# Optimization experiments

Measured on AMD Instinct MI355X. Metric: run time of the kernel, lower is better.

## Reference

```python
import jax, jax.numpy as jnp
import numpy as np

B_, L_, D_ = 8, 2048, 1024      # batch, seq_len, d_model
E, DS, K = 2, 16, 4             # expand, d_state, d_conv
DI = E * D_                     # d_inner = 2048
DTR = (D_ + 15) // 16           # dt_rank = 64


def setup_inputs() -> dict:
    key = jax.random.key(0)
    ks = jax.random.split(key, 8)
    g = lambda k, sh, sc=0.02: jax.random.normal(k, sh, jnp.float32) * sc
    return {
        "x": jax.random.normal(ks[0], (B_, L_, D_), jnp.float32),
        "ln_w": jnp.ones((D_,), jnp.float32),
        "ln_b": jnp.zeros((D_,), jnp.float32),
        "W_in": g(ks[1], (D_, 2 * DI)),
        "conv_w": g(ks[2], (DI, 1, K), 0.1),
        "conv_b": jnp.zeros((DI,), jnp.float32),
        "W_x": g(ks[3], (DI, DTR + 2 * DS)),
        "W_dt": g(ks[4], (DTR, DI), 0.1),
        "b_dt": jnp.full((DI,), -4.0, jnp.float32),  # softplus(-4) ~ 0.018 (small init dt)
        "A_log": jnp.log(jnp.broadcast_to(jnp.arange(1, DS + 1, dtype=jnp.float32), (DI, DS))),
        "Dp": jnp.ones((DI,), jnp.float32),
        "W_out": g(ks[5], (DI, D_)),
    }


def _mamba_block(x, ln_w, ln_b, W_in, conv_w, conv_b, W_x, W_dt, b_dt, A_log, Dp, W_out):
    # pre-norm
    mu = jnp.mean(x, axis=-1, keepdims=True)
    var = jnp.var(x, axis=-1, keepdims=True)
    xn = (x - mu) / jnp.sqrt(var + 1e-5) * ln_w + ln_b

    # input projection -> (u, z), each (B, L, DI)
    xz = jnp.einsum('bld,de->ble', xn, W_in)
    u, z = jnp.split(xz, 2, axis=-1)

    # causal depthwise conv1d along L
    uc = jax.lax.conv_general_dilated(
        u.transpose(0, 2, 1), conv_w, window_strides=(1,), padding=[(K - 1, 0)],
        feature_group_count=DI, dimension_numbers=('NCH', 'OIH', 'NCH'))
    u = jax.nn.silu(uc.transpose(0, 2, 1) + conv_b)

    # input-dependent SSM params
    xd = jnp.einsum('bld,de->ble', u, W_x)          # (B, L, DTR + 2*DS)
    dt = jax.nn.softplus(jnp.einsum('blr,rd->bld', xd[..., :DTR], W_dt) + b_dt)  # (B, L, DI)
    Bm = xd[..., DTR:DTR + DS]                       # (B, L, DS)
    Cm = xd[..., DTR + DS:]                          # (B, L, DS)
    A = -jnp.exp(A_log)                              # (DI, DS)

    # selective scan over time; carry h: (B, DI, DS)
    def step(h, inp):
        dt_t, u_t, B_t, C_t = inp                    # (B,DI),(B,DI),(B,DS),(B,DS)
        dA = jnp.exp(dt_t[..., None] * A)            # (B, DI, DS)
        h = h * dA + (dt_t * u_t)[..., None] * B_t[:, None, :]
        y = jnp.einsum('bds,bs->bd', h, C_t)
        return h, y

    h0 = jnp.zeros((x.shape[0], DI, DS), x.dtype)
    xs = (dt.transpose(1, 0, 2), u.transpose(1, 0, 2), Bm.transpose(1, 0, 2), Cm.transpose(1, 0, 2))
    _, ys = jax.lax.scan(step, h0, xs)               # ys: (L, B, DI)

    y = ys.transpose(1, 0, 2) + u * Dp
    y = y * jax.nn.silu(z)
    # output projection + residual (dropout is identity in eval)
    return jnp.einsum('bld,de->ble', y, W_out) + x


def reference(x, ln_w, ln_b, W_in, conv_w, conv_b, W_x, W_dt, b_dt, A_log, Dp, W_out):
    return _mamba_block(x, ln_w, ln_b, W_in, conv_w, conv_b, W_x, W_dt, b_dt, A_log, Dp, W_out)
```

## Files before the change

### kernel.cpp

```cpp
#include <hip/hip_runtime.h>

#define NB 8
#define NL 2048
#define ND 1024
#define NDI 2048
#define NDS 16
#define NDTR 64
#define NM (NB * NL)
#define CH 16
#define CL (NL / CH)

__device__ __forceinline__ float bf2f(unsigned int u) {
  union { unsigned int i; float f; } c; c.i = u << 16; return c.f;
}
__device__ __forceinline__ float lo16(unsigned int w) { return __uint_as_float(w << 16); }
__device__ __forceinline__ float hi16(unsigned int w) { return __uint_as_float(w & 0xffff0000u); }
__device__ __forceinline__ unsigned short f2bf(float f) {
  unsigned int x = __float_as_uint(f);
  x = x + 0x7fffu + ((x >> 16) & 1u);
  return (unsigned short)(x >> 16);
}
__device__ __forceinline__ void dec8(int4 raw, float* f) {
  f[0] = lo16((unsigned)raw.x); f[1] = hi16((unsigned)raw.x);
  f[2] = lo16((unsigned)raw.y); f[3] = hi16((unsigned)raw.y);
  f[4] = lo16((unsigned)raw.z); f[5] = hi16((unsigned)raw.z);
  f[6] = lo16((unsigned)raw.w); f[7] = hi16((unsigned)raw.w);
}
__device__ __forceinline__ float softplus_fast(float x) {
  return fmaxf(x, 0.f) + __logf(1.f + __expf(-fabsf(x)));
}

typedef __bf16 bf16x8 __attribute__((ext_vector_type(8)));
typedef float f32x4 __attribute__((ext_vector_type(4)));

__device__ __forceinline__ void gld_lds16(const unsigned short* g, unsigned short* l) {
  __builtin_amdgcn_global_load_lds(
      (const __attribute__((address_space(1))) unsigned int*)g,
      (__attribute__((address_space(3))) unsigned int*)l, 16, 0, 0);
}

__global__ __launch_bounds__(256) void k_ln(const float* __restrict__ x,
    const float* __restrict__ lw, const float* __restrict__ lb,
    unsigned short* __restrict__ xn)
{
  const int row = blockIdx.x;
  const int tid = threadIdx.x;
  const float* xr = x + (size_t)row * ND;
  float4 v = reinterpret_cast<const float4*>(xr)[tid];
  float s  = v.x + v.y + v.z + v.w;
  float s2 = v.x*v.x + v.y*v.y + v.z*v.z + v.w*v.w;
  #pragma unroll
  for (int m = 32; m >= 1; m >>= 1) {
    s  += __shfl_xor(s, m);
    s2 += __shfl_xor(s2, m);
  }
  __shared__ float red[8];
  const int wid = tid >> 6;
  if ((tid & 63) == 0) { red[wid] = s; red[4 + wid] = s2; }
  __syncthreads();
  s  = red[0] + red[1] + red[2] + red[3];
  s2 = red[4] + red[5] + red[6] + red[7];
  const float mu   = s * (1.0f / ND);
  const float var  = s2 * (1.0f / ND) - mu * mu;
  const float rstd = rsqrtf(var + 1e-5f);
  const float4 wv = reinterpret_cast<const float4*>(lw)[tid];
  const float4 bv = reinterpret_cast<const float4*>(lb)[tid];
  ushort4 o;
  o.x = f2bf((v.x - mu) * rstd * wv.x + bv.x);
  o.y = f2bf((v.y - mu) * rstd * wv.y + bv.y);
  o.z = f2bf((v.z - mu) * rstd * wv.z + bv.z);
  o.w = f2bf((v.w - mu) * rstd * wv.w + bv.w);
  reinterpret_cast<ushort4*>(xn + (size_t)row * ND)[tid] = o;
}

__global__ __launch_bounds__(256) void k_transpose(
    const float* __restrict__ W, unsigned short* __restrict__ WT,
    const int K, const int N)
{
  __shared__ float t[32][33];
  const int k0 = blockIdx.y * 32, n0 = blockIdx.x * 32;
  const int tx = threadIdx.x & 31, ty = threadIdx.x >> 5;
  #pragma unroll
  for (int r = 0; r < 4; ++r)
    t[ty + r * 8][tx] = W[(size_t)(k0 + ty + r * 8) * N + n0 + tx];
  __syncthreads();
  #pragma unroll
  for (int r = 0; r < 4; ++r)
    WT[(size_t)(n0 + ty + r * 8) * K + k0 + tx] = f2bf(t[tx][ty + r * 8]);
}

template<int MODE>
__global__ __launch_bounds__(512, 2) void k_mfma2(
    const unsigned short* __restrict__ A, const unsigned short* __restrict__ BT,
    const int K, const int N, void* __restrict__ O0, void* __restrict__ O1,
    const float* __restrict__ aux)
{
  __shared__ __align__(16) unsigned short sh[32768];
  const int tid = threadIdx.x, lane = tid & 63, wv = tid >> 6;
  const int wm = wv >> 2, wn = wv & 3;
  const int m16 = lane & 15, kb = lane >> 4;
  const int swzs = (((kb * 16) ^ (((m16 >> 1) & 3) << 4)) >> 1);
  const int arow = wm * 128 + m16;
  const int brow = wn * 64 + m16;

  int wg = blockIdx.x;
  const int cpx = gridDim.x >> 3;
  wg = (wg & 7) * cpx + (wg >> 3);
  const int gnx = N >> 8;
  const int m0 = (wg / gnx) << 8;
  const int n0 = (wg % gnx) << 8;

  f32x4 acc[8][4];
  #pragma unroll
  for (int i = 0; i < 8; ++i)
    #pragma unroll
    for (int j = 0; j < 4; ++j)
      #pragma unroll
      for (int r = 0; r < 4; ++r) acc[i][j][r] = 0.f;

  auto STAGE = [&](const unsigned short* X, int x0, int kg, unsigned short* base) {
    #pragma unroll
    for (int jj = 0; jj < 2; ++jj) {
      const int s = (wv * 2 + jj) * 64 + lane;
      const int row = s >> 2;
      const int c = (lane & 3) ^ ((row >> 1) & 3);
      gld_lds16(X + (size_t)(x0 + row) * K + kg + c * 8, base + (wv * 2 + jj) * 512);
    }
  };
  auto RD_A = [&](bf16x8* dst, const unsigned short* base, int FH) {
    #pragma unroll
    for (int i = 0; i < 4; ++i)
      dst[i] = *reinterpret_cast<const bf16x8*>(base + (arow + FH * 64 + i * 16) * 32 + swzs);
  };
  auto RD_B = [&](bf16x8* dst, const unsigned short* base) {
    #pragma unroll
    for (int j = 0; j < 4; ++j)
      dst[j] = *reinterpret_cast<const bf16x8*>(base + (brow + j * 16) * 32 + swzs);
  };
  auto MM = [&](const bf16x8* aF, const bf16x8* bF, int off) {
    #pragma unroll
    for (int i = 0; i < 4; ++i)
      #pragma unroll
      for (int j = 0; j < 4; ++j)
        acc[off + i][j] = __builtin_amdgcn_mfma_f32_16x16x32_bf16(aF[i], bF[j], acc[off + i][j], 0, 0, 0);
  };

  STAGE(A,  m0, 0, sh);
  STAGE(BT, n0, 0, sh + 8192);
  asm volatile("s_waitcnt vmcnt(0)" ::: "memory");
  __builtin_amdgcn_s_barrier();

  const int NT = K >> 5;
  for (int t = 0; t < NT; ++t) {
    const int buf = t & 1;
    const unsigned short* cA = sh + buf * 16384;
    const unsigned short* cB = cA + 8192;
    unsigned short* nA = sh + (buf ^ 1) * 16384;
    const bool more = (t + 1 < NT);
    if (more) {
      const int kn = (t + 1) << 5;
      STAGE(A,  m0, kn, nA);
      STAGE(BT, n0, kn, nA + 8192);
    }
    bf16x8 a0[4], a1[4], bF[4];
    RD_A(a0, cA, 0);
    RD_B(bF, cB);
    RD_A(a1, cA, 1);
    __builtin_amdgcn_sched_barrier(0);
    __builtin_amdgcn_s_setprio(1);
    MM(a0, bF, 0);
    MM(a1, bF, 4);
    __builtin_amdgcn_s_setprio(0);
    if (more) asm volatile("s_waitcnt vmcnt(0)" ::: "memory");
    __builtin_amdgcn_s_barrier();
  }

  {
    float* fsh = (float*)sh;
    constexpr int LDP = 260;
    const int erow = tid >> 4;
    const int ec0  = tid & 15;
    const int growb = m0 + (erow >> 4) * 128 + (erow & 15);
    #pragma unroll
    for (int i = 0; i < 8; ++i) {
      __builtin_amdgcn_s_barrier();
      #pragma unroll
      for (int j = 0; j < 4; ++j)
        #pragma unroll
        for (int r = 0; r < 4; ++r)
          fsh[(wm * 16 + kb * 4 + r) * LDP + wn * 64 + j * 16 + m16] = acc[i][j][r];
      __builtin_amdgcn_s_barrier();
      const int grow = growb + i * 16;
      #pragma unroll
      for (int q = 0; q < 4; ++q) {
        const int c = (ec0 + q * 16) * 4;
        float4 v = *reinterpret_cast<const float4*>(&fsh[erow * LDP + c]);
        const int colg = n0 + c;
        if constexpr (MODE == 0) {
          ushort4 o = {f2bf(v.x), f2bf(v.y), f2bf(v.z), f2bf(v.w)};
          unsigned short* dst = (colg < NDI)
              ? (unsigned short*)O0 + (size_t)grow * NDI + colg
              : (unsigned short*)O1 + (size_t)grow * NDI + colg - NDI;
          *reinterpret_cast<ushort4*>(dst) = o;
        } else {
          float4 rv = *reinterpret_cast<const float4*>(aux + (size_t)grow * N + colg);
          float4 o = {v.x + rv.x, v.y + rv.y, v.z + rv.z, v.w + rv.w};
          *reinterpret_cast<float4*>((float*)O0 + (size_t)grow * N + colg) = o;
        }
      }
    }
  }
  (void)O1; (void)aux;
}

__global__ __launch_bounds__(256) void k_mfma_dt(
    const unsigned short* __restrict__ A, const unsigned short* __restrict__ BT,
    const int K, void* __restrict__ O0, const float* __restrict__ aux, const int N)
{
  __shared__ __align__(16) unsigned short As[128 * 32];
  __shared__ __align__(16) unsigned short Bs[128 * 32];
  const int tid = threadIdx.x;
  const int lane = tid & 63;
  const int wv = tid >> 6;
  const int wm = wv >> 1, wn = wv & 1;
  const int m0 = blockIdx.y * 128, n0 = blockIdx.x * 128;
  const int m16 = lane & 15, kb = lane >> 4;
  const int wbase = wv * 64;

  f32x4 acc[4][4];
  #pragma unroll
  for (int i = 0; i < 4; ++i)
    #pragma unroll
    for (int j = 0; j < 4; ++j)
      #pragma unroll
      for (int r = 0; r < 4; ++r) acc[i][j][r] = 0.f;

  for (int k0 = 0; k0 < K; k0 += 32) {
    #pragma unroll
    for (int it = 0; it < 2; ++it) {
      const int c = it * 256 + tid;
      const int r = c >> 2, cb = c & 3;
      gld_lds16(A  + (size_t)(m0 + r) * K + k0 + cb * 8, As + (size_t)(it * 256 + wbase) * 8);
      gld_lds16(BT + (size_t)(n0 + r) * K + k0 + cb * 8, Bs + (size_t)(it * 256 + wbase) * 8);
    }
    __syncthreads();
    bf16x8 af[4], bfr[4];
    #pragma unroll
    for (int i = 0; i < 4; ++i)
      af[i] = *reinterpret_cast<const bf16x8*>(&As[(wm * 64 + i * 16 + m16) * 32 + kb * 8]);
    #pragma unroll
    for (int j = 0; j < 4; ++j)
      bfr[j] = *reinterpret_cast<const bf16x8*>(&Bs[(wn * 64 + j * 16 + m16) * 32 + kb * 8]);
    #pragma unroll
    for (int i = 0; i < 4; ++i)
      #pragma unroll
      for (int j = 0; j < 4; ++j)
        acc[i][j] = __builtin_amdgcn_mfma_f32_16x16x32_bf16(af[i], bfr[j], acc[i][j], 0, 0, 0);
    __syncthreads();
  }

  const int r0 = (lane >> 4) * 4;
  #pragma unroll
  for (int i = 0; i < 4; ++i) {
    const int rowb = m0 + wm * 64 + i * 16 + r0;
    #pragma unroll
    for (int j = 0; j < 4; ++j) {
      const int col = n0 + wn * 64 + j * 16 + m16;
      #pragma unroll
      for (int r = 0; r < 4; ++r) {
        const int row = rowb + r;
        ((unsigned short*)O0)[(size_t)row * N + col] =
            f2bf(softplus_fast(acc[i][j][r] + aux[col]));
      }
    }
  }
}

__global__ __launch_bounds__(256) void k_conv(
    const unsigned short* __restrict__ up, const float* __restrict__ cw,
    const float* __restrict__ cb, unsigned short* __restrict__ u)
{
  const int tid = threadIdx.x;
  const int c0 = tid * 8;
  const int lt = blockIdx.x & 127;
  const int b  = blockIdx.x >> 7;
  const int l0 = lt * 16;

  float4 wv[8];
  #pragma unroll
  for (int j = 0; j < 8; ++j)
    wv[j] = reinterpret_cast<const float4*>(cw + (size_t)c0 * 4)[j];
  float bias[8];
  {
    float4 b0 = reinterpret_cast<const float4*>(cb + c0)[0];
    float4 b1 = reinterpret_cast<const float4*>(cb + c0)[1];
    bias[0]=b0.x; bias[1]=b0.y; bias[2]=b0.z; bias[3]=b0.w;
    bias[4]=b1.x; bias[5]=b1.y; bias[6]=b1.z; bias[7]=b1.w;
  }

  const size_t base = ((size_t)b * NL + l0) * NDI + c0;
  float w0[8], w1[8], w2[8];
  if (l0 >= 3) {
    int4 r0 = *reinterpret_cast<const int4*>(up + base - 3 * NDI);
    int4 r1 = *reinterpret_cast<const int4*>(up + base - 2 * NDI);
    int4 r2 = *reinterpret_cast<const int4*>(up + base - 1 * NDI);
    dec8(r0, w0); dec8(r1, w1); dec8(r2, w2);
  } else {
    #pragma unroll
    for (int j = 0; j < 8; ++j) { w0[j] = 0.f; w1[j] = 0.f; w2[j] = 0.f; }
  }

  #pragma unroll
  for (int l = 0; l < 16; ++l) {
    int4 raw = *reinterpret_cast<const int4*>(up + base + (size_t)l * NDI);
    float cur[8];
    dec8(raw, cur);
    unsigned short o[8];
    #pragma unroll
    for (int j = 0; j < 8; ++j) {
      const float a = bias[j] + wv[j].x * w0[j] + wv[j].y * w1[j]
                              + wv[j].z * w2[j] + wv[j].w * cur[j];
      o[j] = f2bf(a / (1.f + __expf(-a)));
    }
    ushort4 o0 = {o[0], o[1], o[2], o[3]};
    ushort4 o1 = {o[4], o[5], o[6], o[7]};
    unsigned short* dst = u + base + (size_t)l * NDI;
    *reinterpret_cast<ushort4*>(dst)     = o0;
    *reinterpret_cast<ushort4*>(dst + 4) = o1;
    #pragma unroll
    for (int j = 0; j < 8; ++j) { w0[j] = w1[j]; w1[j] = w2[j]; w2[j] = cur[j]; }
  }
}

__global__ __launch_bounds__(256) void k_xd_mfma(
    const unsigned short* __restrict__ A, const unsigned short* __restrict__ BT,
    unsigned short* __restrict__ xdt, float* __restrict__ xb,
    float* __restrict__ xc)
{
  __shared__ __align__(16) unsigned short As[2][64 * 32];
  __shared__ __align__(16) unsigned short Bs[2][96 * 32];
  const int tid = threadIdx.x, lane = tid & 63, wvv = tid >> 6;
  const int m0 = blockIdx.x * 64;
  const int m16 = lane & 15, kb = lane >> 4;
  const int sw = (kb ^ ((m16 >> 1) & 3)) * 8;

  f32x4 acc[6];
  #pragma unroll
  for (int j = 0; j < 6; ++j)
    #pragma unroll
    for (int r = 0; r < 4; ++r) acc[j][r] = 0.f;

  auto STG = [&](int bb, int kg) {
    {
      const int row = tid >> 2, c = tid & 3;
      const int sc = c ^ ((row >> 1) & 3);
      gld_lds16(A + (size_t)(m0 + row) * NDI + kg + sc * 8, &As[bb][tid * 8]);
      gld_lds16(BT + (size_t)row * NDI + kg + sc * 8, &Bs[bb][tid * 8]);
    }
    if (tid < 128) {
      const int s = 256 + tid;
      const int row = s >> 2, c = s & 3;
      const int sc = c ^ ((row >> 1) & 3);
      gld_lds16(BT + (size_t)row * NDI + kg + sc * 8, &Bs[bb][s * 8]);
    }
  };

  STG(0, 0);
  asm volatile("s_waitcnt vmcnt(0)" ::: "memory");
  __syncthreads();

  for (int t = 0; t < NDI / 32; ++t) {
    const int cur = t & 1;
    if (t + 1 < NDI / 32) STG(cur ^ 1, (t + 1) * 32);
    bf16x8 af = *reinterpret_cast<const bf16x8*>(&As[cur][(wvv * 16 + m16) * 32 + sw]);
    bf16x8 bfr[6];
    #pragma unroll
    for (int j = 0; j < 6; ++j)
      bfr[j] = *reinterpret_cast<const bf16x8*>(&Bs[cur][(j * 16 + m16) * 32 + sw]);
    #pragma unroll
    for (int j = 0; j < 6; ++j)
      acc[j] = __builtin_amdgcn_mfma_f32_16x16x32_bf16(af, bfr[j], acc[j], 0, 0, 0);
    asm volatile("s_waitcnt vmcnt(0)" ::: "memory");
    __syncthreads();
  }

  const int r0 = kb * 4;
  #pragma unroll
  for (int j = 0; j < 6; ++j) {
    const int col = j * 16 + m16;
    #pragma unroll
    for (int r = 0; r < 4; ++r) {
      const int row = m0 + wvv * 16 + r0 + r;
      const float v = acc[j][r];
      if (j < 4)       xdt[(size_t)row * 64 + col] = f2bf(v);
      else if (j == 4) xb[(size_t)row * 16 + col - 64] = v;
      else             xc[(size_t)row * 16 + col - 80] = v;
    }
  }
}

template<int PHASE>
__global__ __launch_bounds__(256) void k_scan3(
    const unsigned short* __restrict__ dt, unsigned short* __restrict__ u_io,
    const unsigned short* __restrict__ z,
    const float* __restrict__ xb, const float* __restrict__ xc,
    const float* __restrict__ A_log, const float* __restrict__ Dp,
    float* __restrict__ HF, float* __restrict__ Sdt)
{
  const int tid = threadIdx.x;
  const int blk = blockIdx.x;
  const int b = blk >> 7;
  const int c = (blk >> 3) & (CH - 1);
  if (PHASE == 0 && c == CH - 1) return;
  const int d = (blk & 7) * 256 + tid;

  __shared__ float Bsl[CL][16];
  __shared__ float Csl[(PHASE == 1) ? CL : 1][16];
  const size_t rbase = (size_t)b * NL + (size_t)c * CL;
  #pragma unroll
  for (int i = 0; i < 2; ++i) {
    const int idx = i * 256 + tid;
    const int r = idx >> 2, q = idx & 3;
    reinterpret_cast<float4*>(&Bsl[r][q * 4])[0] =
        reinterpret_cast<const float4*>(xb + (rbase + r) * 16)[q];
    if constexpr (PHASE == 1)
      reinterpret_cast<float4*>(&Csl[r][q * 4])[0] =
          reinterpret_cast<const float4*>(xc + (rbase + r) * 16)[q];
  }
  __syncthreads();

  float Ac[16];
  #pragma unroll
  for (int q = 0; q < 4; ++q) {
    float4 a = reinterpret_cast<const float4*>(A_log + (size_t)d * 16)[q];
    Ac[q*4+0] = -__expf(a.x); Ac[q*4+1] = -__expf(a.y);
    Ac[q*4+2] = -__expf(a.z); Ac[q*4+3] = -__expf(a.w);
  }
  bool fastok = true;
  #pragma unroll
  for (int s = 1; s < 16; ++s)
    fastok = fastok && (fabsf(Ac[s] - Ac[0] * (float)(s + 1)) <= 1e-5f * fabsf(Ac[s]));
  const bool fast = __all(fastok);

  const size_t hoff = ((size_t)(b * CH + c) * NDI + d) * 16;
  float h[16];
  if constexpr (PHASE == 0) {
    #pragma unroll
    for (int s = 0; s < 16; ++s) h[s] = 0.f;
  } else {
    #pragma unroll
    for (int q = 0; q < 4; ++q) {
      float4 hv = reinterpret_cast<const float4*>(HF + hoff)[q];
      h[q*4+0] = hv.x; h[q*4+1] = hv.y; h[q*4+2] = hv.z; h[q*4+3] = hv.w;
    }
  }
  const float Dd = Dp[d];
  const float Ac0 = Ac[0];
  float sdt = 0.f;
  size_t idx = rbase * NDI + d;

  if (fast) {
    for (int l = 0; l < CL; ++l, idx += NDI) {
      const float dtv = bf2f(dt[idx]);
      const float uv  = bf2f(u_io[idx]);
      const float dtu = dtv * uv;
      const float qq = __expf(dtv * Ac0);
      float e = qq;
      if constexpr (PHASE == 0) {
        sdt += dtv;
        #pragma unroll
        for (int s = 0; s < 16; ++s) {
          h[s] = h[s] * e + dtu * Bsl[l][s];
          e *= qq;
        }
      } else {
        float yp = 0.f;
        #pragma unroll
        for (int s = 0; s < 16; ++s) {
          h[s] = h[s] * e + dtu * Bsl[l][s];
          yp += h[s] * Csl[l][s];
          e *= qq;
        }
        const float zv = bf2f(z[idx]);
        const float sil = zv / (1.f + __expf(-zv));
        u_io[idx] = f2bf((yp + uv * Dd) * sil);
      }
    }
  } else {
    for (int l = 0; l < CL; ++l, idx += NDI) {
      const float dtv = bf2f(dt[idx]);
      const float uv  = bf2f(u_io[idx]);
      const float dtu = dtv * uv;
      if constexpr (PHASE == 0) {
        sdt += dtv;
        #pragma unroll
        for (int s = 0; s < 16; ++s) {
          const float e = __expf(dtv * Ac[s]);
          h[s] = h[s] * e + dtu * Bsl[l][s];
        }
      } else {
        float yp = 0.f;
        #pragma unroll
        for (int s = 0; s < 16; ++s) {
          const float e = __expf(dtv * Ac[s]);
          h[s] = h[s] * e + dtu * Bsl[l][s];
          yp += h[s] * Csl[l][s];
        }
        const float zv = bf2f(z[idx]);
        const float sil = zv / (1.f + __expf(-zv));
        u_io[idx] = f2bf((yp + uv * Dd) * sil);
      }
    }
  }

  if constexpr (PHASE == 0) {
    #pragma unroll
    for (int q = 0; q < 4; ++q) {
      float4 hv = {h[q*4+0], h[q*4+1], h[q*4+2], h[q*4+3]};
      reinterpret_cast<float4*>(HF + hoff)[q] = hv;
    }
    Sdt[(size_t)(b * CH + c) * NDI + d] = sdt;
  }
}

__global__ __launch_bounds__(256) void k_comb(
    float* __restrict__ HF, const float* __restrict__ Sdt,
    const float* __restrict__ A_log)
{
  const int t = blockIdx.x * 256 + threadIdx.x;
  const int b = t >> 15;
  const int q = t & 32767;
  const int d = q >> 4;
  const float Ac = -__expf(A_log[q]);
  float H = 0.f;
  #pragma unroll
  for (int c = 0; c < CH; ++c) {
    const size_t off = (((size_t)(b * CH + c) * NDI) << 4) + q;
    const float hf = HF[off];
    const float p  = __expf(Ac * Sdt[(size_t)(b * CH + c) * NDI + d]);
    HF[off] = H;
    H = p * H + hf;
  }
}

extern "C" void kernel_launch(void* const* d_in, const int* in_sizes, int n_in,
                              void* d_out, int out_size, void* d_ws, size_t ws_size,
                              hipStream_t stream) {
  (void)in_sizes; (void)n_in; (void)out_size; (void)ws_size;
  const float* x      = (const float*)d_in[0];
  const float* ln_w   = (const float*)d_in[1];
  const float* ln_b   = (const float*)d_in[2];
  const float* W_in   = (const float*)d_in[3];
  const float* conv_w = (const float*)d_in[4];
  const float* conv_b = (const float*)d_in[5];
  const float* W_x    = (const float*)d_in[6];
  const float* W_dt   = (const float*)d_in[7];
  const float* b_dt   = (const float*)d_in[8];
  const float* A_log  = (const float*)d_in[9];
  const float* Dp     = (const float*)d_in[10];
  const float* W_out  = (const float*)d_in[11];
  float* out = (float*)d_out;

  char* ws = (char*)d_ws;
  unsigned short* xn   = (unsigned short*)(ws);
  float*          HF   = (float*)(ws);
  unsigned short* upre = (unsigned short*)(ws + 33554432);
  unsigned short* zbuf = (unsigned short*)(ws + 100663296);
  unsigned short* ubuf = (unsigned short*)(ws + 167772160);
  unsigned short* xdt  = (unsigned short*)(ws + 234881024);
  float*          Sdt  = (float*)(ws + 234881024);
  float*          xb   = (float*)(ws + 236978176);
  float*          xc   = (float*)(ws + 238026752);
  unsigned short* WxT  = (unsigned short*)(ws + 239075328);
  unsigned short* WdtT = (unsigned short*)(ws + 239468544);
  unsigned short* WinT = (unsigned short*)(ws + 240123904);
  unsigned short* WoutT= (unsigned short*)(ws + 248512512);

  dim3 gt1(4096 / 32, 1024 / 32);
  k_transpose<<<gt1, 256, 0, stream>>>(W_in, WinT, 1024, 4096);
  dim3 gt2(1024 / 32, 2048 / 32);
  k_transpose<<<gt2, 256, 0, stream>>>(W_out, WoutT, 2048, 1024);
  dim3 gt3(96 / 32, 2048 / 32);
  k_transpose<<<gt3, 256, 0, stream>>>(W_x, WxT, 2048, 96);
  dim3 gt4(2048 / 32, 64 / 32);
  k_transpose<<<gt4, 256, 0, stream>>>(W_dt, WdtT, 64, 2048);

  k_ln<<<NM, 256, 0, stream>>>(x, ln_w, ln_b, xn);

  k_mfma2<0><<<(NM / 256) * (4096 / 256), 512, 0, stream>>>(
      xn, WinT, 1024, 4096, upre, zbuf, nullptr);

  k_conv<<<NB * (NL / 16), 256, 0, stream>>>(upre, conv_w, conv_b, ubuf);

  k_xd_mfma<<<NM / 64, 256, 0, stream>>>(ubuf, WxT, xdt, xb, xc);

  dim3 g3(2048 / 128, NM / 128);
  k_mfma_dt<<<g3, 256, 0, stream>>>(xdt, WdtT, 64, upre, b_dt, 2048);

  const int nscan = NB * CH * (NDI / 256);
  k_scan3<0><<<nscan, 256, 0, stream>>>(upre, ubuf, zbuf, xb, xc, A_log, Dp, HF, Sdt);
  k_comb<<<NB * NDI * NDS / 256, 256, 0, stream>>>(HF, Sdt, A_log);
  k_scan3<1><<<nscan, 256, 0, stream>>>(upre, ubuf, zbuf, xb, xc, A_log, Dp, HF, Sdt);

  k_mfma2<1><<<(NM / 256) * (1024 / 256), 512, 0, stream>>>(
      ubuf, WoutT, 2048, 1024, out, nullptr, x);
}
```

Before: 540.8 us.

## Shrink GEMM tile to 128x256 for higher occupancy and coalesce dt epilogue

The main bf16 MFMA GEMM moves from a 256x256 tile to a 128x256 tile. This halves the accumulator registers and cuts LDS per block, so launch bounds rise to four blocks per CU and the grid doubles. In exchange each block reuses its staged B data across fewer rows, so arithmetic intensity drops. The dt-projection kernel's epilogue now goes through shared memory and writes vectorized ushort4 rows instead of scattered 2-byte stores, at the cost of extra barriers and LDS.

Result: no change. 550.4 us (+1.8%).

```diff
diff --git a/kernel.cpp b/kernel.cpp
--- a/kernel.cpp
+++ b/kernel.cpp
@@ -90,86 +90,81 @@
 }
 
 template<int MODE>
-__global__ __launch_bounds__(512, 2) void k_mfma2(
+__global__ __launch_bounds__(512, 4) void k_mfma3(
     const unsigned short* __restrict__ A, const unsigned short* __restrict__ BT,
     const int K, const int N, void* __restrict__ O0, void* __restrict__ O1,
     const float* __restrict__ aux)
 {
-  __shared__ __align__(16) unsigned short sh[32768];
+  __shared__ __align__(16) unsigned short sh[24576];
   const int tid = threadIdx.x, lane = tid & 63, wv = tid >> 6;
   const int wm = wv >> 2, wn = wv & 3;
   const int m16 = lane & 15, kb = lane >> 4;
   const int swzs = (((kb * 16) ^ (((m16 >> 1) & 3) << 4)) >> 1);
-  const int arow = wm * 128 + m16;
+  const int arow = wm * 64 + m16;
   const int brow = wn * 64 + m16;
 
   int wg = blockIdx.x;
   const int cpx = gridDim.x >> 3;
   wg = (wg & 7) * cpx + (wg >> 3);
   const int gnx = N >> 8;
-  const int m0 = (wg / gnx) << 8;
+  const int m0 = (wg / gnx) << 7;
   const int n0 = (wg % gnx) << 8;
 
-  f32x4 acc[8][4];
-  #pragma unroll
-  for (int i = 0; i < 8; ++i)
+  f32x4 acc[4][4];
+  #pragma unroll
+  for (int i = 0; i < 4; ++i)
     #pragma unroll
     for (int j = 0; j < 4; ++j)
       #pragma unroll
       for (int r = 0; r < 4; ++r) acc[i][j][r] = 0.f;
 
-  auto STAGE = [&](const unsigned short* X, int x0, int kg, unsigned short* base) {
+  auto STAGE_A = [&](int kg, unsigned short* base) {
+    const int s = wv * 64 + lane;
+    const int row = s >> 2;
+    const int c = (s & 3) ^ ((row >> 1) & 3);
+    gld_lds16(A + (size_t)(m0 + row) * K + kg + c * 8, base + wv * 512);
+  };
+  auto STAGE_B = [&](int kg, unsigned short* base) {
     #pragma unroll
     for (int jj = 0; jj < 2; ++jj) {
       const int s = (wv * 2 + jj) * 64 + lane;
       const int row = s >> 2;
-      const int c = (lane & 3) ^ ((row >> 1) & 3);
-      gld_lds16(X + (size_t)(x0 + row) * K + kg + c * 8, base + (wv * 2 + jj) * 512);
+      const int c = (s & 3) ^ ((row >> 1) & 3);
+      gld_lds16(BT + (size_t)(n0 + row) * K + kg + c * 8, base + (wv * 2 + jj) * 512);
     }
   };
-  auto RD_A = [&](bf16x8* dst, const unsigned short* base, int FH) {
-    #pragma unroll
-    for (int i = 0; i < 4; ++i)
-      dst[i] = *reinterpret_cast<const bf16x8*>(base + (arow + FH * 64 + i * 16) * 32 + swzs);
-  };
-  auto RD_B = [&](bf16x8* dst, const unsigned short* base) {
-    #pragma unroll
-    for (int j = 0; j < 4; ++j)
-      dst[j] = *reinterpret_cast<const bf16x8*>(base + (brow + j * 16) * 32 + swzs);
-  };
-  auto MM = [&](const bf16x8* aF, const bf16x8* bF, int off) {
-    #pragma unroll
-    for (int i = 0; i < 4; ++i)
-      #pragma unroll
-      for (int j = 0; j < 4; ++j)
-        acc[off + i][j] = __builtin_amdgcn_mfma_f32_16x16x32_bf16(aF[i], bF[j], acc[off + i][j], 0, 0, 0);
-  };
-
-  STAGE(A,  m0, 0, sh);
-  STAGE(BT, n0, 0, sh + 8192);
+
+  STAGE_A(0, sh);
+  STAGE_B(0, sh + 4096);
   asm volatile("s_waitcnt vmcnt(0)" ::: "memory");
   __builtin_amdgcn_s_barrier();
 
   const int NT = K >> 5;
   for (int t = 0; t < NT; ++t) {
     const int buf = t & 1;
-    const unsigned short* cA = sh + buf * 16384;
-    const unsigned short* cB = cA + 8192;
-    unsigned short* nA = sh + (buf ^ 1) * 16384;
+    const unsigned short* cA = sh + buf * 12288;
+    const unsigned short* cB = cA + 4096;
+    unsigned short* nBuf = sh + (buf ^ 1) * 12288;
     const bool more = (t + 1 < NT);
     if (more) {
       const int kn = (t + 1) << 5;
-      STAGE(A,  m0, kn, nA);
-      STAGE(BT, n0, kn, nA + 8192);
-    }
-    bf16x8 a0[4], a1[4], bF[4];
-    RD_A(a0, cA, 0);
-    RD_B(bF, cB);
-    RD_A(a1, cA, 1);
+      STAGE_A(kn, nBuf);
+      STAGE_B(kn, nBuf + 4096);
+    }
+    bf16x8 aF[4], bF[4];
+    #pragma unroll
+    for (int i = 0; i < 4; ++i)
+      aF[i] = *reinterpret_cast<const bf16x8*>(cA + (arow + i * 16) * 32 + swzs);
+    #pragma unroll
+    for (int j = 0; j < 4; ++j)
+      bF[j] = *reinterpret_cast<const bf16x8*>(cB + (brow + j * 16) * 32 + swzs);
     __builtin_amdgcn_sched_barrier(0);
     __builtin_amdgcn_s_setprio(1);
-    MM(a0, bF, 0);
-    MM(a1, bF, 4);
+    #pragma unroll
+    for (int i = 0; i < 4; ++i)
+      #pragma unroll
+      for (int j = 0; j < 4; ++j)
+        acc[i][j] = __builtin_amdgcn_mfma_f32_16x16x32_bf16(aF[i], bF[j], acc[i][j], 0, 0, 0);
     __builtin_amdgcn_s_setprio(0);
     if (more) asm volatile("s_waitcnt vmcnt(0)" ::: "memory");
     __builtin_amdgcn_s_barrier();
@@ -180,9 +175,8 @@
     constexpr int LDP = 260;
     const int erow = tid >> 4;
     const int ec0  = tid & 15;
-    const int growb = m0 + (erow >> 4) * 128 + (erow & 15);
-    #pragma unroll
-    for (int i = 0; i < 8; ++i) {
+    #pragma unroll
+    for (int i = 0; i < 4; ++i) {
       __builtin_amdgcn_s_barrier();
       #pragma unroll
       for (int j = 0; j < 4; ++j)
@@ -190,7 +184,7 @@
         for (int r = 0; r < 4; ++r)
           fsh[(wm * 16 + kb * 4 + r) * LDP + wn * 64 + j * 16 + m16] = acc[i][j][r];
       __builtin_amdgcn_s_barrier();
-      const int grow = growb + i * 16;
+      const int grow = m0 + (erow >> 4) * 64 + i * 16 + (erow & 15);
       #pragma unroll
       for (int q = 0; q < 4; ++q) {
         const int c = (ec0 + q * 16) * 4;
@@ -219,6 +213,7 @@
 {
   __shared__ __align__(16) unsigned short As[128 * 32];
   __shared__ __align__(16) unsigned short Bs[128 * 32];
+  __shared__ __align__(16) float fshd[32 * 132];
   const int tid = threadIdx.x;
   const int lane = tid & 63;
   const int wv = tid >> 6;
@@ -259,18 +254,31 @@
     __syncthreads();
   }
 
-  const int r0 = (lane >> 4) * 4;
-  #pragma unroll
-  for (int i = 0; i < 4; ++i) {
-    const int rowb = m0 + wm * 64 + i * 16 + r0;
-    #pragma unroll
-    for (int j = 0; j < 4; ++j) {
-      const int col = n0 + wn * 64 + j * 16 + m16;
-      #pragma unroll
-      for (int r = 0; r < 4; ++r) {
-        const int row = rowb + r;
-        ((unsigned short*)O0)[(size_t)row * N + col] =
-            f2bf(softplus_fast(acc[i][j][r] + aux[col]));
+  {
+    constexpr int LDP = 132;
+    const int erow = tid >> 3;
+    const int ec0  = tid & 7;
+    #pragma unroll
+    for (int i = 0; i < 4; ++i) {
+      __syncthreads();
+      #pragma unroll
+      for (int j = 0; j < 4; ++j)
+        #pragma unroll
+        for (int r = 0; r < 4; ++r)
+          fshd[(wm * 16 + kb * 4 + r) * LDP + wn * 64 + j * 16 + m16] = acc[i][j][r];
+      __syncthreads();
+      const int grow = m0 + (erow >> 4) * 64 + i * 16 + (erow & 15);
+      #pragma unroll
+      for (int q = 0; q < 4; ++q) {
+        const int c = (ec0 + q * 8) * 4;
+        float4 v = *reinterpret_cast<const float4*>(&fshd[erow * LDP + c]);
+        const int colg = n0 + c;
+        ushort4 o;
+        o.x = f2bf(softplus_fast(v.x + aux[colg + 0]));
+        o.y = f2bf(softplus_fast(v.y + aux[colg + 1]));
+        o.z = f2bf(softplus_fast(v.z + aux[colg + 2]));
+        o.w = f2bf(softplus_fast(v.w + aux[colg + 3]));
+        *reinterpret_cast<ushort4*>((unsigned short*)O0 + (size_t)grow * N + colg) = o;
       }
     }
   }
@@ -587,7 +595,7 @@
 
   k_ln<<<NM, 256, 0, stream>>>(x, ln_w, ln_b, xn);
 
-  k_mfma2<0><<<(NM / 256) * (4096 / 256), 512, 0, stream>>>(
+  k_mfma3<0><<<(NM / 128) * (4096 / 256), 512, 0, stream>>>(
       xn, WinT, 1024, 4096, upre, zbuf, nullptr);
 
   k_conv<<<NB * (NL / 16), 256, 0, stream>>>(upre, conv_w, conv_b, ubuf);
@@ -602,6 +610,6 @@
   k_comb<<<NB * NDI * NDS / 256, 256, 0, stream>>>(HF, Sdt, A_log);
   k_scan3<1><<<nscan, 256, 0, stream>>>(upre, ubuf, zbuf, xb, xc, A_log, Dp, HF, Sdt);
 
-  k_mfma2<1><<<(NM / 256) * (1024 / 256), 512, 0, stream>>>(
+  k_mfma3<1><<<(NM / 128) * (1024 / 256), 512, 0, stream>>>(
       ubuf, WoutT, 2048, 1024, out, nullptr, x);
 }
```
